# Performance work log

Measured on AMD Instinct MI355X. Metric: run time of the kernel, lower is better.

Reference implementation:

```python
import jax, jax.numpy as jnp
import numpy as np

DMAX = 32
TEMPERATURE = 1.0

B, C, H, T, F = 2, 64, 64, 512, 64


def _windows(x, dmax):
    """x: (..., T, F) -> (..., T, dmax, F); w[..., t, d, :] = x_padded[..., t + d, :],
    where x is zero-padded with dmax-1 frames at the front of T (causal window
    covering frames t-dmax+1 .. t, matching torch ZeroPad2d+Unfold)."""
    Tn = x.shape[-2]
    pad = [(0, 0)] * (x.ndim - 2) + [(dmax - 1, 0), (0, 0)]
    xp = jnp.pad(x, pad)
    idx = jnp.arange(Tn)[:, None] + jnp.arange(dmax)[None, :]  # (T, dmax)
    return xp[..., idx, :]


def setup_inputs() -> dict:
    key = jax.random.key(0)
    ks = jax.random.split(key, 8)
    return {
        "x_mic": jax.random.normal(ks[0], (B, C, T, F), dtype=jnp.float32),
        "x_ref": jax.random.normal(ks[1], (B, C, T, F), dtype=jnp.float32),
        "w_mic": jax.random.normal(ks[2], (H, C), dtype=jnp.float32) * (1.0 / np.sqrt(C)),
        "b_mic": jax.random.normal(ks[3], (H,), dtype=jnp.float32) * 0.01,
        "w_ref": jax.random.normal(ks[4], (H, C), dtype=jnp.float32) * (1.0 / np.sqrt(C)),
        "b_ref": jax.random.normal(ks[5], (H,), dtype=jnp.float32) * 0.01,
        "w_conv": jax.random.normal(ks[6], (1, H, 5, 3), dtype=jnp.float32) * (1.0 / np.sqrt(H * 15)),
        "b_conv": jax.random.normal(ks[7], (1,), dtype=jnp.float32) * 0.01,
    }


def reference(x_mic, x_ref, w_mic, b_mic, w_ref, b_ref, w_conv, b_conv):
    Bn, Cn, Tn, Fn = x_ref.shape
    # 1x1 convs == channel-mixing matmuls
    Q = jnp.einsum('bctf,hc->bhtf', x_mic, w_mic) + b_mic[None, :, None, None]
    K = jnp.einsum('bctf,hc->bhtf', x_ref, w_ref) + b_ref[None, :, None, None]
    # causal sliding windows over T: (B,H,T,dmax,F)
    Kw = _windows(K, DMAX)
    # cross-correlation scores over F: (B,H,T,dmax)
    V = jnp.einsum('bhtf,bhtdf->bhtd', Q, Kw) / jnp.sqrt(jnp.asarray(Fn, jnp.float32))
    # conv over (T, dmax): pad T top by 4 (causal), dmax both sides by 1; kernel (5,3), H->1
    Vp = jnp.pad(V, ((0, 0), (0, 0), (4, 0), (1, 1)))
    Vc = jax.lax.conv_general_dilated(
        Vp, w_conv, window_strides=(1, 1), padding='VALID',
        dimension_numbers=('NCHW', 'OIHW', 'NCHW')) + b_conv[None, :, None, None]
    # delay distribution over dmax
    A = jax.nn.softmax(Vc / TEMPERATURE, axis=-1)  # (B,1,T,dmax)
    # align reference: weighted sum over the causal window
    refw = _windows(x_ref, DMAX)  # (B,C,T,dmax,F)
    aligned = jnp.einsum('btd,bctdf->bctf', A[:, 0], refw)
    return aligned
```

## Files before the change

kernel.cpp:

```cpp
#include <hip/hip_runtime.h>
#include <hip/hip_bf16.h>

#define BB 2
#define CC 64
#define HH 64
#define TT 512
#define FF 64
#define DD 32

typedef short short8 __attribute__((ext_vector_type(8)));
typedef float f32x4  __attribute__((ext_vector_type(4)));

__device__ __forceinline__ unsigned short f2bf(float x) {
    union { float f; unsigned u; } v; v.f = x;
    unsigned r = v.u + 0x7FFFu + ((v.u >> 16) & 1u);
    return (unsigned short)(r >> 16);
}

__global__ __launch_bounds__(256) void k_qk(
    const float* __restrict__ x_mic, const float* __restrict__ x_ref,
    const float* __restrict__ w_mic, const float* __restrict__ b_mic,
    const float* __restrict__ w_ref, const float* __restrict__ b_ref,
    unsigned short* __restrict__ Qb, unsigned short* __restrict__ Kb)
{
    __shared__ unsigned short Wl[64 * 72];
    __shared__ unsigned short Xt[2][64 * 72];
    __shared__ float Bs[64];

    const int tid = threadIdx.x;
    const int b   = blockIdx.x >> 8;
    const int t0  = (blockIdx.x & 255) * 2;
    const int which = blockIdx.y;

    const float* xsrc = which ? x_ref : x_mic;
    const float* wsrc = which ? w_ref : w_mic;
    const float* bsrc = which ? b_ref : b_mic;
    unsigned short* outb = which ? Kb : Qb;

    const int l  = tid & 63;
    const int w  = tid >> 6;
    const int q  = l >> 4;
    const int nl = l & 15;

    {
        const float4* wg = reinterpret_cast<const float4*>(wsrc);
        const int h  = tid >> 2;
        #pragma unroll
        for (int p = 0; p < 4; ++p) {
            const int c0 = (tid & 3) * 4 + p * 16;
            float4 wv = wg[h * 16 + (c0 >> 2)];
            unsigned w0 = (unsigned)f2bf(wv.x) | ((unsigned)f2bf(wv.y) << 16);
            unsigned w1 = (unsigned)f2bf(wv.z) | ((unsigned)f2bf(wv.w) << 16);
            uint2* dst = reinterpret_cast<uint2*>(&Wl[h * 72 + c0]);
            *dst = make_uint2(w0, w1);
        }
    }
    if (tid < 64) Bs[tid] = bsrc[tid];

    {
        const float4* xg = reinterpret_cast<const float4*>(
            xsrc + (size_t)b * CC * TT * FF);
        #pragma unroll
        for (int t = 0; t < 2; ++t) {
            #pragma unroll
            for (int p = 0; p < 4; ++p) {
                const int cbase = p * 16 + 4 * w;
                const int c     = cbase + q;
                float4 xv = xg[((size_t)c * TT + (t0 + t)) * 16 + nl];
                float v0 = xv.x, v1 = xv.y, v2 = xv.z, v3 = xv.w;
                float s01 = __shfl_xor((q & 1) ? v0 : v1, 16);
                float s23 = __shfl_xor((q & 1) ? v2 : v3, 16);
                float w0 = (q & 1) ? s01 : v0;
                float w1 = (q & 1) ? v1  : s01;
                float w2 = (q & 1) ? s23 : v2;
                float w3 = (q & 1) ? v3  : s23;
                float r02 = __shfl_xor((q & 2) ? w0 : w2, 32);
                float r13 = __shfl_xor((q & 2) ? w1 : w3, 32);
                float u0 = (q & 2) ? r02 : w0;
                float u1 = (q & 2) ? r13 : w1;
                float u2 = (q & 2) ? w2  : r02;
                float u3 = (q & 2) ? w3  : r13;
                unsigned a0 = (unsigned)f2bf(u0) | ((unsigned)f2bf(u1) << 16);
                unsigned a1 = (unsigned)f2bf(u2) | ((unsigned)f2bf(u3) << 16);
                uint2* dst = reinterpret_cast<uint2*>(
                    &Xt[t][(4 * nl + q) * 72 + cbase]);
                *dst = make_uint2(a0, a1);
            }
        }
    }
    __syncthreads();

    short8 b0 = *reinterpret_cast<const short8*>(&Wl[(16 * w + nl) * 72 + q * 8]);
    short8 b1 = *reinterpret_cast<const short8*>(&Wl[(16 * w + nl) * 72 + (4 + q) * 8]);
    const int h = 16 * w + nl;
    const float bv = Bs[h];

    #pragma unroll
    for (int t = 0; t < 2; ++t) {
        #pragma unroll
        for (int mt = 0; mt < 4; ++mt) {
            f32x4 acc = (f32x4){0.f, 0.f, 0.f, 0.f};
            short8 a0 = *reinterpret_cast<const short8*>(
                &Xt[t][(16 * mt + nl) * 72 + q * 8]);
            short8 a1 = *reinterpret_cast<const short8*>(
                &Xt[t][(16 * mt + nl) * 72 + (4 + q) * 8]);
            acc = __builtin_amdgcn_mfma_f32_16x16x32_bf16(a0, b0, acc, 0, 0, 0);
            acc = __builtin_amdgcn_mfma_f32_16x16x32_bf16(a1, b1, acc, 0, 0, 0);
            unsigned lo = (unsigned)f2bf(acc[0] + bv) | ((unsigned)f2bf(acc[1] + bv) << 16);
            unsigned hi = (unsigned)f2bf(acc[2] + bv) | ((unsigned)f2bf(acc[3] + bv) << 16);
            uint2* dst = reinterpret_cast<uint2*>(
                &outb[((size_t)(b * HH + h) * TT + (t0 + t)) * FF + 16 * mt + 4 * q]);
            *dst = make_uint2(lo, hi);
        }
    }
}

__global__ __launch_bounds__(256) void k_scores(
    const unsigned short* __restrict__ Qb, const unsigned short* __restrict__ Kb,
    float* __restrict__ V)
{
    __shared__ unsigned short Ql[64 * 72];
    __shared__ unsigned short Kl[96 * 72];

    const int tid = threadIdx.x;
    const int t0  = blockIdx.x * 64;
    const int h   = blockIdx.y, b = blockIdx.z;

    const size_t base = ((size_t)(b * HH + h) * TT) * FF;

    #pragma unroll
    for (int it = 0; it < 5; ++it) {
        int idx = it * 256 + tid;
        if (idx < 512) {
            int r = idx >> 3, g = idx & 7;
            uint4 v = *reinterpret_cast<const uint4*>(Qb + base + (size_t)(t0 + r) * FF + g * 8);
            *reinterpret_cast<uint4*>(&Ql[r * 72 + g * 8]) = v;
        } else {
            int idx2 = idx - 512;
            int r = idx2 >> 3, g = idx2 & 7;
            int j = t0 - 31 + r;
            uint4 v = make_uint4(0u, 0u, 0u, 0u);
            if (j >= 0 && j < TT)
                v = *reinterpret_cast<const uint4*>(Kb + base + (size_t)j * FF + g * 8);
            *reinterpret_cast<uint4*>(&Kl[r * 72 + g * 8]) = v;
        }
    }
    __syncthreads();

    const int l = tid & 63;
    const int w = tid >> 6;
    const int q = l >> 4;
    const int nl = l & 15;

    short8 a0 = *reinterpret_cast<const short8*>(&Ql[(16 * w + nl) * 72 + q * 8]);
    short8 a1 = *reinterpret_cast<const short8*>(&Ql[(16 * w + nl) * 72 + (4 + q) * 8]);

    f32x4 acc[3];
    #pragma unroll
    for (int n = 0; n < 3; ++n) acc[n] = (f32x4){0.f, 0.f, 0.f, 0.f};

    #pragma unroll
    for (int n = 0; n < 3; ++n) {
        short8 b0 = *reinterpret_cast<const short8*>(
            &Kl[(16 * w + 16 * n + nl) * 72 + q * 8]);
        short8 b1 = *reinterpret_cast<const short8*>(
            &Kl[(16 * w + 16 * n + nl) * 72 + (4 + q) * 8]);
        acc[n] = __builtin_amdgcn_mfma_f32_16x16x32_bf16(a0, b0, acc[n], 0, 0, 0);
        acc[n] = __builtin_amdgcn_mfma_f32_16x16x32_bf16(a1, b1, acc[n], 0, 0, 0);
    }

    #pragma unroll
    for (int n = 0; n < 3; ++n) {
        #pragma unroll
        for (int r = 0; r < 4; ++r) {
            const int tloc = 16 * w + 4 * q + r;
            const int d = 16 * n + nl - 4 * q - r;
            if (d >= 0 && d < DD) {
                const int t = t0 + tloc;
                V[((size_t)(b * TT + t) * HH + h) * DD + d] = acc[n][r] * 0.125f;
            }
        }
    }
}

__global__ __launch_bounds__(256) void k_conv_softmax(
    const float* __restrict__ V, const float* __restrict__ wconv,
    const float* __restrict__ bconv, float* __restrict__ A)
{
    __shared__ float Vs[8 * 2304];
    __shared__ float wcs[960];

    const int tid = threadIdx.x;
    const int t0 = blockIdx.x * 4, b = blockIdx.y;

    #pragma unroll
    for (int idx = tid; idx < 960; idx += 256) wcs[idx] = wconv[idx];

    const float4* vg = reinterpret_cast<const float4*>(V);
    #pragma unroll
    for (int it = 0; it < 16; ++it) {
        int idx = it * 256 + tid;
        int r = idx >> 9, g = idx & 511;
        int h = g >> 3, d4 = g & 7;
        int tt = t0 - 4 + r;
        float4 v = make_float4(0.f, 0.f, 0.f, 0.f);
        if (tt >= 0) v = vg[((size_t)(b * TT) + tt) * 512 + g];
        *reinterpret_cast<float4*>(&Vs[r * 2304 + h * 36 + d4 * 4]) = v;
    }
    __syncthreads();

    const int dq = tid & 7;
    const int hg = (tid >> 3) & 7;
    const int tt = tid >> 6;

    float px = 0.f, py = 0.f, pz = 0.f, pw = 0.f;
    #pragma unroll
    for (int i = 0; i < 5; ++i) {
        const int r = tt + i;
        #pragma unroll
        for (int hh = 0; hh < 8; ++hh) {
            const int h = hg + 8 * hh;
            float4 cur = *reinterpret_cast<const float4*>(
                &Vs[r * 2304 + h * 36 + dq * 4]);
            float pv = __shfl_up(cur.w, 1);
            float nx = __shfl_down(cur.x, 1);
            if (dq == 0) pv = 0.f;
            if (dq == 7) nx = 0.f;
            const float w0 = wcs[h * 15 + i * 3 + 0];
            const float w1 = wcs[h * 15 + i * 3 + 1];
            const float w2 = wcs[h * 15 + i * 3 + 2];
            px += w0 * pv    + w1 * cur.x + w2 * cur.y;
            py += w0 * cur.x + w1 * cur.y + w2 * cur.z;
            pz += w0 * cur.y + w1 * cur.z + w2 * cur.w;
            pw += w0 * cur.z + w1 * cur.w + w2 * nx;
        }
    }
    #pragma unroll
    for (int off = 8; off <= 32; off <<= 1) {
        px += __shfl_xor(px, off);
        py += __shfl_xor(py, off);
        pz += __shfl_xor(pz, off);
        pw += __shfl_xor(pw, off);
    }
    const float bc = bconv[0];
    px += bc; py += bc; pz += bc; pw += bc;
    float m = fmaxf(fmaxf(px, py), fmaxf(pz, pw));
    #pragma unroll
    for (int off = 1; off <= 4; off <<= 1) m = fmaxf(m, __shfl_xor(m, off));
    float ex = __expf(px - m), ey = __expf(py - m);
    float ez = __expf(pz - m), ew = __expf(pw - m);
    float s = ex + ey + ez + ew;
    #pragma unroll
    for (int off = 1; off <= 4; off <<= 1) s += __shfl_xor(s, off);
    const float inv = 1.f / s;
    if (hg == 0) {
        const int t = t0 + tt;
        float4 av = make_float4(ex * inv, ey * inv, ez * inv, ew * inv);
        *reinterpret_cast<float4*>(&A[((size_t)(b * TT) + t) * DD + 4 * dq]) = av;
    }
}

__global__ __launch_bounds__(256) void k_align(
    const float* __restrict__ x_ref, const float* __restrict__ A, float* __restrict__ out)
{
    __shared__ float Xs[95 * 68];
    __shared__ float As[64 * 36];
    __shared__ float Ap[16 * 37 * 4];

    const int tid = threadIdx.x;
    const int t0  = blockIdx.x * 64;
    const int c   = blockIdx.y, b = blockIdx.z;

    const float4* xg = reinterpret_cast<const float4*>(
        x_ref + ((size_t)(b * CC + c) * TT) * FF);
    float4* xs4 = reinterpret_cast<float4*>(Xs);
    #pragma unroll
    for (int it = 0; it < 6; ++it) {
        int idx = it * 256 + tid;
        if (idx < 95 * 16) {
            int r = idx >> 4, f4 = idx & 15;
            int tt = t0 - 31 + r;
            float4 v = make_float4(0.f, 0.f, 0.f, 0.f);
            if (tt >= 0) v = xg[tt * 16 + f4];
            xs4[r * 17 + f4] = v;
        }
    }
    #pragma unroll
    for (int it = 0; it < 2; ++it) {
        int idx = it * 256 + tid;
        int i = idx >> 3, d4 = idx & 7;
        *reinterpret_cast<float4*>(&As[i * 36 + 4 * d4]) =
            *reinterpret_cast<const float4*>(&A[((size_t)(b * TT) + t0 + i) * DD + 4 * d4]);
    }
    __syncthreads();
    #pragma unroll
    for (int it = 0; it < 3; ++it) {
        int idx = it * 256 + tid;
        if (idx < 16 * 37) {
            int bi = idx / 37, rr = idx - bi * 37;
            float wv[4];
            #pragma unroll
            for (int r = 0; r < 4; ++r) {
                int d = rr - r;
                wv[r] = (d >= 0 && d < 32) ? As[(4 * bi + r) * 36 + d] : 0.f;
            }
            float4* dst = reinterpret_cast<float4*>(&Ap[(bi * 37 + rr) * 4]);
            *dst = make_float4(wv[0], wv[1], wv[2], wv[3]);
        }
    }
    __syncthreads();

    const int f4 = tid & 15;
    const int bi = tid >> 4;

    float4 acc0 = make_float4(0.f, 0.f, 0.f, 0.f);
    float4 acc1 = make_float4(0.f, 0.f, 0.f, 0.f);
    float4 acc2 = make_float4(0.f, 0.f, 0.f, 0.f);
    float4 acc3 = make_float4(0.f, 0.f, 0.f, 0.f);

    #pragma unroll 7
    for (int rr = 0; rr < 35; ++rr) {
        float4 W4 = *reinterpret_cast<const float4*>(&Ap[(bi * 37 + rr) * 4]);
        float4 X4 = xs4[(4 * bi + rr) * 17 + f4];
        acc0.x += W4.x * X4.x; acc0.y += W4.x * X4.y; acc0.z += W4.x * X4.z; acc0.w += W4.x * X4.w;
        acc1.x += W4.y * X4.x; acc1.y += W4.y * X4.y; acc1.z += W4.y * X4.z; acc1.w += W4.y * X4.w;
        acc2.x += W4.z * X4.x; acc2.y += W4.z * X4.y; acc2.z += W4.z * X4.z; acc2.w += W4.z * X4.w;
        acc3.x += W4.w * X4.x; acc3.y += W4.w * X4.y; acc3.z += W4.w * X4.z; acc3.w += W4.w * X4.w;
    }

    float4* o4 = reinterpret_cast<float4*>(out);
    const size_t obase = ((size_t)(b * CC + c) * TT + t0 + 4 * bi) * 16 + f4;
    o4[obase +  0] = acc0;
    o4[obase + 16] = acc1;
    o4[obase + 32] = acc2;
    o4[obase + 48] = acc3;
}

extern "C" void kernel_launch(void* const* d_in, const int* in_sizes, int n_in,
                              void* d_out, int out_size, void* d_ws, size_t ws_size,
                              hipStream_t stream)
{
    const float* x_mic  = (const float*)d_in[0];
    const float* x_ref  = (const float*)d_in[1];
    const float* w_mic  = (const float*)d_in[2];
    const float* b_mic  = (const float*)d_in[3];
    const float* w_ref  = (const float*)d_in[4];
    const float* b_ref  = (const float*)d_in[5];
    const float* w_conv = (const float*)d_in[6];
    const float* b_conv = (const float*)d_in[7];
    float* out = (float*)d_out;

    unsigned short* Qb = (unsigned short*)d_ws;
    unsigned short* Kb = Qb + 4194304;
    float* V = (float*)(Kb + 4194304);
    float* A = V + 2097152;

    k_qk<<<dim3(BB * (TT / 2), 2), 256, 0, stream>>>(
        x_mic, x_ref, w_mic, b_mic, w_ref, b_ref, Qb, Kb);
    k_scores<<<dim3(TT / 64, HH, BB), 256, 0, stream>>>(Qb, Kb, V);
    k_conv_softmax<<<dim3(TT / 4, BB), 256, 0, stream>>>(V, w_conv, b_conv, A);
    k_align<<<dim3(TT / 64, CC, BB), 256, 0, stream>>>(x_ref, A, out);
}
```

Before: 125.7 us.

## Use split-bf16 MFMA in align kernel, widen qk tiles, pad conv smem

The align kernel's scalar FP32 FMA loop is replaced by an MFMA bf16 matmul. x_ref is split into high and low bf16 parts so precision stays near fp32, and the softmax weights are expanded into a banded bf16 matrix. Separately, the Q/K projection kernel now handles four time steps per block instead of two, and the conv kernel pads its shared buffer so neighbour values are read from LDS instead of through shuffles. Rounding the softmax weights A to bf16 adds error to the output.

```diff
diff --git a/kernel.cpp b/kernel.cpp
--- a/kernel.cpp
+++ b/kernel.cpp
@@ -15,6 +15,10 @@
     union { float f; unsigned u; } v; v.f = x;
     unsigned r = v.u + 0x7FFFu + ((v.u >> 16) & 1u);
     return (unsigned short)(r >> 16);
+}
+__device__ __forceinline__ float bf2f(unsigned short h) {
+    union { unsigned u; float f; } v; v.u = ((unsigned)h) << 16;
+    return v.f;
 }
 
 __global__ __launch_bounds__(256) void k_qk(
@@ -24,12 +28,12 @@
     unsigned short* __restrict__ Qb, unsigned short* __restrict__ Kb)
 {
     __shared__ unsigned short Wl[64 * 72];
-    __shared__ unsigned short Xt[2][64 * 72];
+    __shared__ unsigned short Xt[4][64 * 72];
     __shared__ float Bs[64];
 
     const int tid = threadIdx.x;
-    const int b   = blockIdx.x >> 8;
-    const int t0  = (blockIdx.x & 255) * 2;
+    const int b   = blockIdx.x >> 7;
+    const int t0  = (blockIdx.x & 127) * 4;
     const int which = blockIdx.y;
 
     const float* xsrc = which ? x_ref : x_mic;
@@ -61,7 +65,7 @@
         const float4* xg = reinterpret_cast<const float4*>(
             xsrc + (size_t)b * CC * TT * FF);
         #pragma unroll
-        for (int t = 0; t < 2; ++t) {
+        for (int t = 0; t < 4; ++t) {
             #pragma unroll
             for (int p = 0; p < 4; ++p) {
                 const int cbase = p * 16 + 4 * w;
@@ -96,7 +100,7 @@
     const float bv = Bs[h];
 
     #pragma unroll
-    for (int t = 0; t < 2; ++t) {
+    for (int t = 0; t < 4; ++t) {
         #pragma unroll
         for (int mt = 0; mt < 4; ++mt) {
             f32x4 acc = (f32x4){0.f, 0.f, 0.f, 0.f};
@@ -187,7 +191,7 @@
     const float* __restrict__ V, const float* __restrict__ wconv,
     const float* __restrict__ bconv, float* __restrict__ A)
 {
-    __shared__ float Vs[8 * 2304];
+    __shared__ float Vs[8 * 2304 + 8];
     __shared__ float wcs[960];
 
     const int tid = threadIdx.x;
@@ -195,6 +199,14 @@
 
     #pragma unroll
     for (int idx = tid; idx < 960; idx += 256) wcs[idx] = wconv[idx];
+    if (tid == 0) *reinterpret_cast<float4*>(&Vs[0]) = make_float4(0.f, 0.f, 0.f, 0.f);
+    #pragma unroll
+    for (int it = 0; it < 2; ++it) {
+        int idx = it * 256 + tid;
+        int r = idx >> 6, h = idx & 63;
+        *reinterpret_cast<float4*>(&Vs[4 + r * 2304 + h * 36 + 32]) =
+            make_float4(0.f, 0.f, 0.f, 0.f);
+    }
 
     const float4* vg = reinterpret_cast<const float4*>(V);
     #pragma unroll
@@ -205,7 +217,7 @@
         int tt = t0 - 4 + r;
         float4 v = make_float4(0.f, 0.f, 0.f, 0.f);
         if (tt >= 0) v = vg[((size_t)(b * TT) + tt) * 512 + g];
-        *reinterpret_cast<float4*>(&Vs[r * 2304 + h * 36 + d4 * 4]) = v;
+        *reinterpret_cast<float4*>(&Vs[4 + r * 2304 + h * 36 + d4 * 4]) = v;
     }
     __syncthreads();
 
@@ -220,12 +232,10 @@
         #pragma unroll
         for (int hh = 0; hh < 8; ++hh) {
             const int h = hg + 8 * hh;
-            float4 cur = *reinterpret_cast<const float4*>(
-                &Vs[r * 2304 + h * 36 + dq * 4]);
-            float pv = __shfl_up(cur.w, 1);
-            float nx = __shfl_down(cur.x, 1);
-            if (dq == 0) pv = 0.f;
-            if (dq == 7) nx = 0.f;
+            const int base = 4 + r * 2304 + h * 36 + dq * 4;
+            float4 cur = *reinterpret_cast<const float4*>(&Vs[base]);
+            float pv = Vs[base - 1];
+            float nx = Vs[base + 4];
             const float w0 = wcs[h * 15 + i * 3 + 0];
             const float w1 = wcs[h * 15 + i * 3 + 1];
             const float w2 = wcs[h * 15 + i * 3 + 2];
@@ -263,77 +273,106 @@
 __global__ __launch_bounds__(256) void k_align(
     const float* __restrict__ x_ref, const float* __restrict__ A, float* __restrict__ out)
 {
-    __shared__ float Xs[95 * 68];
-    __shared__ float As[64 * 36];
-    __shared__ float Ap[16 * 37 * 4];
+    __shared__ unsigned short XtH[64 * 96];
+    __shared__ unsigned short XtL[64 * 96];
+    __shared__ unsigned short Ab[64 * 96];
+    __shared__ float As[64 * 32];
 
     const int tid = threadIdx.x;
     const int t0  = blockIdx.x * 64;
     const int c   = blockIdx.y, b = blockIdx.z;
 
-    const float4* xg = reinterpret_cast<const float4*>(
-        x_ref + ((size_t)(b * CC + c) * TT) * FF);
-    float4* xs4 = reinterpret_cast<float4*>(Xs);
-    #pragma unroll
-    for (int it = 0; it < 6; ++it) {
-        int idx = it * 256 + tid;
-        if (idx < 95 * 16) {
-            int r = idx >> 4, f4 = idx & 15;
-            int tt = t0 - 31 + r;
-            float4 v = make_float4(0.f, 0.f, 0.f, 0.f);
-            if (tt >= 0) v = xg[tt * 16 + f4];
-            xs4[r * 17 + f4] = v;
-        }
-    }
-    #pragma unroll
-    for (int it = 0; it < 2; ++it) {
-        int idx = it * 256 + tid;
-        int i = idx >> 3, d4 = idx & 7;
-        *reinterpret_cast<float4*>(&As[i * 36 + 4 * d4]) =
-            *reinterpret_cast<const float4*>(&A[((size_t)(b * TT) + t0 + i) * DD + 4 * d4]);
+    const int l  = tid & 63;
+    const int w  = tid >> 6;
+    const int q  = l >> 4;
+    const int nl = l & 15;
+
+    {
+        const float4* ag = reinterpret_cast<const float4*>(A);
+        #pragma unroll
+        for (int it = 0; it < 2; ++it) {
+            int idx = it * 256 + tid;
+            int i = idx >> 3, d4 = idx & 7;
+            *reinterpret_cast<float4*>(&As[i * 32 + 4 * d4]) =
+                ag[((size_t)(b * TT) + t0 + i) * 8 + d4];
+        }
+    }
+
+    {
+        const float4* xg = reinterpret_cast<const float4*>(
+            x_ref + ((size_t)(b * CC + c) * TT) * FF);
+        #pragma unroll
+        for (int it = 0; it < 6; ++it) {
+            const int jbase = it * 16 + 4 * w;
+            const int j  = jbase + q;
+            const int jg = t0 - 31 + j;
+            float4 xv = make_float4(0.f, 0.f, 0.f, 0.f);
+            if (jg >= 0 && jg < TT) xv = xg[(size_t)jg * 16 + nl];
+            float v0 = xv.x, v1 = xv.y, v2 = xv.z, v3 = xv.w;
+            float s01 = __shfl_xor((q & 1) ? v0 : v1, 16);
+            float s23 = __shfl_xor((q & 1) ? v2 : v3, 16);
+            float w0 = (q & 1) ? s01 : v0;
+            float w1 = (q & 1) ? v1  : s01;
+            float w2 = (q & 1) ? s23 : v2;
+            float w3 = (q & 1) ? v3  : s23;
+            float r02 = __shfl_xor((q & 2) ? w0 : w2, 32);
+            float r13 = __shfl_xor((q & 2) ? w1 : w3, 32);
+            float u0 = (q & 2) ? r02 : w0;
+            float u1 = (q & 2) ? r13 : w1;
+            float u2 = (q & 2) ? w2  : r02;
+            float u3 = (q & 2) ? w3  : r13;
+            unsigned short h0 = f2bf(u0), h1 = f2bf(u1), h2 = f2bf(u2), h3 = f2bf(u3);
+            unsigned short g0 = f2bf(u0 - bf2f(h0)), g1 = f2bf(u1 - bf2f(h1));
+            unsigned short g2 = f2bf(u2 - bf2f(h2)), g3 = f2bf(u3 - bf2f(h3));
+            const int row = (4 * nl + q) * 96 + jbase;
+            *reinterpret_cast<uint2*>(&XtH[row]) =
+                make_uint2((unsigned)h0 | ((unsigned)h1 << 16),
+                           (unsigned)h2 | ((unsigned)h3 << 16));
+            *reinterpret_cast<uint2*>(&XtL[row]) =
+                make_uint2((unsigned)g0 | ((unsigned)g1 << 16),
+                           (unsigned)g2 | ((unsigned)g3 << 16));
+        }
     }
     __syncthreads();
-    #pragma unroll
-    for (int it = 0; it < 3; ++it) {
-        int idx = it * 256 + tid;
-        if (idx < 16 * 37) {
-            int bi = idx / 37, rr = idx - bi * 37;
-            float wv[4];
-            #pragma unroll
-            for (int r = 0; r < 4; ++r) {
-                int d = rr - r;
-                wv[r] = (d >= 0 && d < 32) ? As[(4 * bi + r) * 36 + d] : 0.f;
-            }
-            float4* dst = reinterpret_cast<float4*>(&Ap[(bi * 37 + rr) * 4]);
-            *dst = make_float4(wv[0], wv[1], wv[2], wv[3]);
+
+    {
+        unsigned* ab32 = reinterpret_cast<unsigned*>(Ab);
+        #pragma unroll
+        for (int it = 0; it < 12; ++it) {
+            int idx = it * 256 + tid;
+            int tl = idx / 48, jl2 = idx - tl * 48;
+            int d0 = 2 * jl2 - tl;
+            int d1 = d0 + 1;
+            float w0 = (d0 >= 0 && d0 < 32) ? As[tl * 32 + d0] : 0.f;
+            float w1 = (d1 >= 0 && d1 < 32) ? As[tl * 32 + d1] : 0.f;
+            ab32[tl * 48 + jl2] = (unsigned)f2bf(w0) | ((unsigned)f2bf(w1) << 16);
         }
     }
     __syncthreads();
 
-    const int f4 = tid & 15;
-    const int bi = tid >> 4;
-
-    float4 acc0 = make_float4(0.f, 0.f, 0.f, 0.f);
-    float4 acc1 = make_float4(0.f, 0.f, 0.f, 0.f);
-    float4 acc2 = make_float4(0.f, 0.f, 0.f, 0.f);
-    float4 acc3 = make_float4(0.f, 0.f, 0.f, 0.f);
-
-    #pragma unroll 7
-    for (int rr = 0; rr < 35; ++rr) {
-        float4 W4 = *reinterpret_cast<const float4*>(&Ap[(bi * 37 + rr) * 4]);
-        float4 X4 = xs4[(4 * bi + rr) * 17 + f4];
-        acc0.x += W4.x * X4.x; acc0.y += W4.x * X4.y; acc0.z += W4.x * X4.z; acc0.w += W4.x * X4.w;
-        acc1.x += W4.y * X4.x; acc1.y += W4.y * X4.y; acc1.z += W4.y * X4.z; acc1.w += W4.y * X4.w;
-        acc2.x += W4.z * X4.x; acc2.y += W4.z * X4.y; acc2.z += W4.z * X4.z; acc2.w += W4.z * X4.w;
-        acc3.x += W4.w * X4.x; acc3.y += W4.w * X4.y; acc3.z += W4.w * X4.z; acc3.w += W4.w * X4.w;
+    f32x4 acc[4];
+    #pragma unroll
+    for (int n = 0; n < 4; ++n) acc[n] = (f32x4){0.f, 0.f, 0.f, 0.f};
+
+    #pragma unroll
+    for (int kt = 0; kt < 3; ++kt) {
+        const int k0 = 32 * kt + 8 * q;
+        short8 aH = *reinterpret_cast<const short8*>(&XtH[(16 * w + nl) * 96 + k0]);
+        short8 aL = *reinterpret_cast<const short8*>(&XtL[(16 * w + nl) * 96 + k0]);
+        #pragma unroll
+        for (int n = 0; n < 4; ++n) {
+            short8 bA = *reinterpret_cast<const short8*>(&Ab[(16 * n + nl) * 96 + k0]);
+            acc[n] = __builtin_amdgcn_mfma_f32_16x16x32_bf16(aH, bA, acc[n], 0, 0, 0);
+            acc[n] = __builtin_amdgcn_mfma_f32_16x16x32_bf16(aL, bA, acc[n], 0, 0, 0);
+        }
     }
 
     float4* o4 = reinterpret_cast<float4*>(out);
-    const size_t obase = ((size_t)(b * CC + c) * TT + t0 + 4 * bi) * 16 + f4;
-    o4[obase +  0] = acc0;
-    o4[obase + 16] = acc1;
-    o4[obase + 32] = acc2;
-    o4[obase + 48] = acc3;
+    #pragma unroll
+    for (int n = 0; n < 4; ++n) {
+        const size_t row = (size_t)(b * CC + c) * TT + t0 + 16 * n + nl;
+        o4[row * 16 + 4 * w + q] = make_float4(acc[n][0], acc[n][1], acc[n][2], acc[n][3]);
+    }
 }
 
 extern "C" void kernel_launch(void* const* d_in, const int* in_sizes, int n_in,
@@ -355,7 +394,7 @@
     float* V = (float*)(Kb + 4194304);
     float* A = V + 2097152;
 
-    k_qk<<<dim3(BB * (TT / 2), 2), 256, 0, stream>>>(
+    k_qk<<<dim3(BB * (TT / 4), 2), 256, 0, stream>>>(
         x_mic, x_ref, w_mic, b_mic, w_ref, b_ref, Qb, Kb);
     k_scores<<<dim3(TT / 64, HH, BB), 256, 0, stream>>>(Qb, Kb, V);
     k_conv_softmax<<<dim3(TT / 4, BB), 256, 0, stream>>>(V, w_conv, b_conv, A);
```

After: 130.3 us. 1.04x slower.
